# Optimization experiments

Measured on AMD Instinct MI355X. Metric: run time of the kernel, lower is better.

## Reference

```python
import jax, jax.numpy as jnp
import numpy as np

E = 64          # num_routed_experts
K = 6           # num_experts_per_token
NS = 2          # num_shared_experts
D = 512         # hidden_size
F = 512         # expert_intermediate_size = intermediate_size // 4


def setup_inputs() -> dict:
    key = jax.random.key(0)
    ks = jax.random.split(key, 8)
    s = 0.02
    return {
        "hidden_states": jax.random.normal(ks[0], (2, 1024, D), dtype=jnp.float32),
        "Wr": jax.random.normal(ks[1], (D, E), dtype=jnp.float32) * s,      # router
        "sWg": jax.random.normal(ks[2], (NS, D, F), dtype=jnp.float32) * s,  # shared gate_proj
        "sWu": jax.random.normal(ks[3], (NS, D, F), dtype=jnp.float32) * s,  # shared up_proj
        "sWd": jax.random.normal(ks[4], (NS, F, D), dtype=jnp.float32) * s,  # shared down_proj
        "Wg": jax.random.normal(ks[5], (E, D, F), dtype=jnp.float32) * s,    # routed gate_proj
        "Wu": jax.random.normal(ks[6], (E, D, F), dtype=jnp.float32) * s,    # routed up_proj
        "Wd": jax.random.normal(ks[7], (E, F, D), dtype=jnp.float32) * s,    # routed down_proj
    }


def _swiglu_ffn(x, wg, wu, wd):
    # x: (N, D); wg/wu: (D, F); wd: (F, D)
    return (jax.nn.silu(x @ wg) * (x @ wu)) @ wd


def reference(hidden_states, Wr, sWg, sWu, sWd, Wg, Wu, Wd):
    B, S, d = hidden_states.shape
    x = hidden_states.reshape(-1, d)  # (N, D)
    N = x.shape[0]

    # ---- shared experts (always on) ----
    shared = jnp.zeros_like(x)
    for e in range(NS):
        shared = shared + _swiglu_ffn(x, sWg[e], sWu[e], sWd[e])

    # ---- top-k router ----
    logits = x @ Wr                                   # (N, E)
    probs = jax.nn.softmax(logits, axis=-1)
    top_w, top_i = jax.lax.top_k(probs, K)            # (N, K)
    top_w = top_w / jnp.sum(top_w, axis=-1, keepdims=True)  # renormalize
    gate = jnp.zeros((N, E), dtype=x.dtype).at[jnp.arange(N)[:, None], top_i].set(top_w)

    # ---- routed experts: per-expert FFN, combined with sparse gate ----
    routed = jnp.zeros_like(x)
    for e in range(E):
        routed = routed + _swiglu_ffn(x, Wg[e], Wu[e], Wd[e]) * gate[:, e:e + 1]

    out = (shared + routed + x).reshape(B, S, d)
    return out
```

## Files before the change

### kernel.cpp

```cpp
#include <hip/hip_runtime.h>

#define N_TOK 2048
#define DD 512
#define FF 512
#define EE 64
#define TK 6
#define NG 66
#define RSLOT 12288
#define NSLOT 16384
#define BM 64
#define BN 64
#define NKT2 16
#define MAXT 320
#define MATSZ 262144

typedef float f32x4 __attribute__((ext_vector_type(4)));
typedef __bf16 bf16x8 __attribute__((ext_vector_type(8)));

__device__ __forceinline__ unsigned cvtpk(float lo, float hi) {
  unsigned r;
  asm("v_cvt_pk_bf16_f32 %0, %1, %2" : "=v"(r) : "v"(lo), "v"(hi));
  return r;
}

__device__ __forceinline__ int swz4(int r) { return (r + (r >> 2)) & 3; }

__device__ __forceinline__ void gll16(const void* g, void* l) {
  __builtin_amdgcn_global_load_lds(
      (const __attribute__((address_space(1))) unsigned int*)g,
      (__attribute__((address_space(3))) unsigned int*)l, 16, 0, 0);
}

__device__ __forceinline__ void fence_barrier() {
  asm volatile("" ::: "memory");
  __builtin_amdgcn_s_barrier();
  __builtin_amdgcn_sched_barrier(0);
}

__global__ __launch_bounds__(256) void convw_k(
    const float* __restrict__ Wg, const float* __restrict__ Wu, const float* __restrict__ Wd,
    const float* __restrict__ sWg, const float* __restrict__ sWu, const float* __restrict__ sWd,
    short* __restrict__ Wt) {
  __shared__ float T[64][33];
  int y = blockIdx.y;
  int kind = y / 66, idx = y % 66;
  const float* src;
  if (kind == 0)      src = (idx < EE) ? Wg + (size_t)idx * MATSZ : sWg + (size_t)(idx - EE) * MATSZ;
  else if (kind == 1) src = (idx < EE) ? Wu + (size_t)idx * MATSZ : sWu + (size_t)(idx - EE) * MATSZ;
  else                src = (idx < EE) ? Wd + (size_t)idx * MATSZ : sWd + (size_t)(idx - EE) * MATSZ;
  short* dst = Wt + (size_t)y * MATSZ;
  int d0 = (blockIdx.x & 7) * 64;
  int f0 = (blockIdx.x >> 3) * 32;
  int t = threadIdx.x;

  int r = t >> 3, fo = (t & 7) * 4;
  const float* sp = src + (size_t)(d0 + r) * 512 + f0 + fo;
  *(f32x4*)&T[r][fo]      = *(const f32x4*)sp;
  *(f32x4*)&T[r + 32][fo] = *(const f32x4*)(sp + (size_t)32 * 512);
  __syncthreads();

  int f = t >> 3, a = t & 7, dd = a * 8;
  float v[8];
#pragma unroll
  for (int i = 0; i < 8; ++i) v[i] = T[dd + i][f];
  uint4 o;
  o.x = cvtpk(v[0], v[1]); o.y = cvtpk(v[2], v[3]);
  o.z = cvtpk(v[4], v[5]); o.w = cvtpk(v[6], v[7]);
  *(uint4*)&dst[(size_t)(f0 + f) * 512 + d0 + dd] = o;
}

__global__ void convx_k(const float* __restrict__ x, short* __restrict__ Xb) {
  int i = blockIdx.x * 256 + threadIdx.x;
  const f32x4* p = (const f32x4*)(x + (size_t)i * 8);
  f32x4 v0 = p[0], v1 = p[1];
  uint4 o;
  o.x = cvtpk(v0[0], v0[1]); o.y = cvtpk(v0[2], v0[3]);
  o.z = cvtpk(v1[0], v1[1]); o.w = cvtpk(v1[2], v1[3]);
  *(uint4*)&Xb[(size_t)i * 8] = o;
}

__global__ __launch_bounds__(256) void router_k(
    const float* __restrict__ x, const float* __restrict__ Wr,
    int* __restrict__ top_i, float* __restrict__ top_w, int* __restrict__ cnt) {
  __shared__ float xs[16 * 512];
  __shared__ float part[4][16][64];
  int tid = threadIdx.x, lane = tid & 63, w = tid >> 6;
  int t0 = blockIdx.x * 16;
  const f32x4* xin = (const f32x4*)(x + (size_t)t0 * DD);
  f32x4* xs4 = (f32x4*)xs;
#pragma unroll
  for (int i = 0; i < 8; ++i) xs4[i * 256 + tid] = xin[i * 256 + tid];
  __syncthreads();
  float acc[16];
#pragma unroll
  for (int t = 0; t < 16; ++t) acc[t] = 0.f;
  for (int kk = 0; kk < 32; ++kk) {
    int k = w * 128 + kk * 4;
    float w0 = Wr[(size_t)(k + 0) * EE + lane];
    float w1 = Wr[(size_t)(k + 1) * EE + lane];
    float w2 = Wr[(size_t)(k + 2) * EE + lane];
    float w3 = Wr[(size_t)(k + 3) * EE + lane];
#pragma unroll
    for (int t = 0; t < 16; ++t) {
      f32x4 xv = *(const f32x4*)&xs[t * 512 + k];
      acc[t] = fmaf(xv[0], w0, acc[t]);
      acc[t] = fmaf(xv[1], w1, acc[t]);
      acc[t] = fmaf(xv[2], w2, acc[t]);
      acc[t] = fmaf(xv[3], w3, acc[t]);
    }
  }
#pragma unroll
  for (int t = 0; t < 16; ++t) part[w][t][lane] = acc[t];
  __syncthreads();
#pragma unroll
  for (int tt = 0; tt < 4; ++tt) {
    int t = w * 4 + tt;
    float l0 = part[0][t][lane] + part[1][t][lane] + part[2][t][lane] + part[3][t][lane];
    float m = l0;
#pragma unroll
    for (int s = 32; s; s >>= 1) m = fmaxf(m, __shfl_xor(m, s));
    float p = __expf(l0 - m);
    int wi[TK]; float wv[TK];
#pragma unroll
    for (int it = 0; it < TK; ++it) {
      float v = p;
#pragma unroll
      for (int s = 32; s; s >>= 1) v = fmaxf(v, __shfl_xor(v, s));
      unsigned long long b = __ballot(p == v);
      int idx = __ffsll((unsigned long long)b) - 1;
      wi[it] = idx; wv[it] = v;
      if (lane == idx) p = -1.f;
    }
    float wsum = 0.f;
#pragma unroll
    for (int it = 0; it < TK; ++it) wsum += wv[it];
    int tg = t0 + t;
    if (lane < TK) {
      int si = 0; float sv = 0.f;
#pragma unroll
      for (int it = 0; it < TK; ++it) if (lane == it) { si = wi[it]; sv = wv[it]; }
      top_i[tg * TK + lane] = si;
      top_w[tg * TK + lane] = sv / wsum;
      atomicAdd(&cnt[si], 1);
    }
  }
}

__global__ void offsets_k(const int* __restrict__ cnt, int* __restrict__ goff,
                          int* __restrict__ fill, int* __restrict__ wk_g,
                          int* __restrict__ wk_mt, int* __restrict__ nitems) {
  int i = threadIdx.x;
  fill[i] = 0;
  int c = cnt[i];
  int s = c;
#pragma unroll
  for (int d = 1; d < 64; d <<= 1) { int t = __shfl_up(s, d); if (i >= d) s += t; }
  goff[i] = s - c;
  if (i == 63) {
    goff[EE] = RSLOT;
    goff[EE + 1] = RSLOT + N_TOK;
    goff[EE + 2] = RSLOT + 2 * N_TOK;
  }
  int nt = (c + BM - 1) >> 6;
  int ts = nt;
#pragma unroll
  for (int d = 1; d < 64; d <<= 1) { int t = __shfl_up(ts, d); if (i >= d) ts += t; }
  int texcl = ts - nt;
  for (int t = 0; t < nt; ++t) { wk_g[texcl + t] = i; wk_mt[texcl + t] = t; }
  int tot = __shfl(ts, 63);
  wk_g[tot + i] = EE + (i >> 5);
  wk_mt[tot + i] = i & 31;
  if (i == 0) nitems[0] = tot + 64;
}

__global__ void scatter_k(const int* __restrict__ top_i, const float* __restrict__ top_w,
                          const int* __restrict__ goff, int* __restrict__ fill,
                          int* __restrict__ btok, float* __restrict__ bw,
                          int* __restrict__ tslot) {
  int idx = blockIdx.x * blockDim.x + threadIdx.x;
  if (idx < RSLOT) {
    int e = top_i[idx];
    int pos = goff[e] + atomicAdd(&fill[e], 1);
    btok[pos] = idx / TK;
    bw[pos] = top_w[idx];
    tslot[idx] = pos;
  } else if (idx < NSLOT) {
    int j = idx - RSLOT;
    btok[idx] = j & (N_TOK - 1);
    bw[idx] = 1.0f;
  }
}

__global__ __launch_bounds__(256) void gemm1_k(
    const short* __restrict__ Xb, const short* __restrict__ Wtg, const short* __restrict__ Wtu,
    const int* __restrict__ goff, const int* __restrict__ btok,
    const int* __restrict__ wk_g, const int* __restrict__ wk_mt,
    const int* __restrict__ nitems, short* __restrict__ H) {
  int item = blockIdx.y;
  if (item >= nitems[0]) return;
  int g = wk_g[item], mt = wk_mt[item];
  int s0g = goff[g], cnt = goff[g + 1] - s0g;
  int n0 = blockIdx.x * BN;
  const short* gmat = Wtg + (size_t)g * MATSZ;
  const short* umat = Wtu + (size_t)g * MATSZ;

  __shared__ __align__(16) short lds[2][6144];

  int tid = threadIdx.x, lane = tid & 63, w = tid >> 6;
  int wr = w >> 1, wc = w & 1;
  int lr = lane & 15, lgq = lane >> 4;
  int s0 = s0g + mt * BM;

  const short* sp[3];
  int ldst[3];
#pragma unroll
  for (int q = 0; q < 3; ++q) {
    int c = w * 3 + q;
    int mat = c >> 2, cc = c & 3;
    ldst[q] = mat * 2048 + cc * 512;
    int rl = cc * 16 + (lane >> 2);
    int gu = (lane & 3) ^ swz4(rl);
    if (mat == 0) {
      int slot = (mt * BM + rl < cnt) ? s0 + rl : s0;
      sp[q] = Xb + (size_t)btok[slot] * 512 + gu * 8;
    } else if (mat == 1) {
      sp[q] = gmat + (size_t)(n0 + rl) * 512 + gu * 8;
    } else {
      sp[q] = umat + (size_t)(n0 + rl) * 512 + gu * 8;
    }
  }

  f32x4 accg[2][2], accu[2][2];
#pragma unroll
  for (int i = 0; i < 2; ++i)
#pragma unroll
    for (int j = 0; j < 2; ++j) {
      accg[i][j] = f32x4{0.f, 0.f, 0.f, 0.f};
      accu[i][j] = f32x4{0.f, 0.f, 0.f, 0.f};
    }

  auto STAGE = [&](int b, int kt) {
#pragma unroll
    for (int q = 0; q < 3; ++q) gll16(sp[q] + kt * 32, &lds[b][ldst[q]]);
  };
  auto COMPUTE = [&](int b) {
    const short* L = lds[b];
    bf16x8 af[2], bg[2], bu[2];
#pragma unroll
    for (int i = 0; i < 2; ++i) {
      int row = wr * 32 + i * 16 + lr;
      af[i] = *(const bf16x8*)&L[row * 32 + ((lgq ^ swz4(row)) * 8)];
    }
#pragma unroll
    for (int j = 0; j < 2; ++j) {
      int fr = wc * 32 + j * 16 + lr;
      int o = fr * 32 + ((lgq ^ swz4(fr)) * 8);
      bg[j] = *(const bf16x8*)&L[2048 + o];
      bu[j] = *(const bf16x8*)&L[4096 + o];
    }
#pragma unroll
    for (int i = 0; i < 2; ++i)
#pragma unroll
      for (int j = 0; j < 2; ++j) {
        accg[i][j] = __builtin_amdgcn_mfma_f32_16x16x32_bf16(af[i], bg[j], accg[i][j], 0, 0, 0);
        accu[i][j] = __builtin_amdgcn_mfma_f32_16x16x32_bf16(af[i], bu[j], accu[i][j], 0, 0, 0);
      }
  };

  STAGE(0, 0);
  asm volatile("s_waitcnt vmcnt(0)" ::: "memory");
  fence_barrier();
#pragma unroll 1
  for (int kt = 0; kt < NKT2; ++kt) {
    int cur = kt & 1;
    if (kt + 1 < NKT2) STAGE(cur ^ 1, kt + 1);
    COMPUTE(cur);
    if (kt + 1 < NKT2) asm volatile("s_waitcnt vmcnt(0)" ::: "memory");
    fence_barrier();
  }

#pragma unroll
  for (int i = 0; i < 2; ++i)
#pragma unroll
    for (int j = 0; j < 2; ++j)
#pragma unroll
      for (int r = 0; r < 4; ++r) {
        int mrow = wr * 32 + i * 16 + lgq * 4 + r;
        if (mt * BM + mrow < cnt) {
          float gg = accg[i][j][r];
          float uu = accu[i][j][r];
          float hv = (gg / (1.f + __expf(-gg))) * uu;
          int col = n0 + wc * 32 + j * 16 + lr;
          H[(size_t)(s0 + mrow) * FF + col] = (short)(cvtpk(hv, hv) & 0xffffu);
        }
      }
}

__global__ __launch_bounds__(256) void gemm2_k(
    const short* __restrict__ H, const short* __restrict__ Wtd,
    const int* __restrict__ goff, const float* __restrict__ bw,
    const int* __restrict__ wk_g, const int* __restrict__ wk_mt,
    const int* __restrict__ nitems, short* __restrict__ Osl) {
  int item = blockIdx.y;
  if (item >= nitems[0]) return;
  int g = wk_g[item], mt = wk_mt[item];
  int s0g = goff[g], cnt = goff[g + 1] - s0g;
  int n0 = blockIdx.x * BN;
  const short* dmat = Wtd + (size_t)g * MATSZ;

  __shared__ __align__(16) short lds[2][4096];

  int tid = threadIdx.x, lane = tid & 63, w = tid >> 6;
  int wr = w >> 1, wc = w & 1;
  int lr = lane & 15, lgq = lane >> 4;
  int s0 = s0g + mt * BM;

  const short* sp[2];
  int ldst[2];
#pragma unroll
  for (int q = 0; q < 2; ++q) {
    int c = w * 2 + q;
    int mat = c >> 2, cc = c & 3;
    ldst[q] = mat * 2048 + cc * 512;
    int rl = cc * 16 + (lane >> 2);
    int gu = (lane & 3) ^ swz4(rl);
    if (mat == 0) {
      int slot = (mt * BM + rl < cnt) ? s0 + rl : s0;
      sp[q] = H + (size_t)slot * 512 + gu * 8;
    } else {
      sp[q] = dmat + (size_t)(n0 + rl) * 512 + gu * 8;
    }
  }

  f32x4 acc[2][2];
#pragma unroll
  for (int i = 0; i < 2; ++i)
#pragma unroll
    for (int j = 0; j < 2; ++j) acc[i][j] = f32x4{0.f, 0.f, 0.f, 0.f};

  auto STAGE = [&](int b, int kt) {
#pragma unroll
    for (int q = 0; q < 2; ++q) gll16(sp[q] + kt * 32, &lds[b][ldst[q]]);
  };
  auto COMPUTE = [&](int b) {
    const short* L = lds[b];
    bf16x8 af[2], bd[2];
#pragma unroll
    for (int i = 0; i < 2; ++i) {
      int row = wr * 32 + i * 16 + lr;
      af[i] = *(const bf16x8*)&L[row * 32 + ((lgq ^ swz4(row)) * 8)];
    }
#pragma unroll
    for (int j = 0; j < 2; ++j) {
      int dr = wc * 32 + j * 16 + lr;
      bd[j] = *(const bf16x8*)&L[2048 + dr * 32 + ((lgq ^ swz4(dr)) * 8)];
    }
#pragma unroll
    for (int i = 0; i < 2; ++i)
#pragma unroll
      for (int j = 0; j < 2; ++j)
        acc[i][j] = __builtin_amdgcn_mfma_f32_16x16x32_bf16(af[i], bd[j], acc[i][j], 0, 0, 0);
  };

  STAGE(0, 0);
  asm volatile("s_waitcnt vmcnt(0)" ::: "memory");
  fence_barrier();
#pragma unroll 1
  for (int kt = 0; kt < NKT2; ++kt) {
    int cur = kt & 1;
    if (kt + 1 < NKT2) STAGE(cur ^ 1, kt + 1);
    COMPUTE(cur);
    if (kt + 1 < NKT2) asm volatile("s_waitcnt vmcnt(0)" ::: "memory");
    fence_barrier();
  }

#pragma unroll
  for (int i = 0; i < 2; ++i)
#pragma unroll
    for (int r = 0; r < 4; ++r) {
      int mrow = wr * 32 + i * 16 + lgq * 4 + r;
      if (mt * BM + mrow < cnt) {
        int slot = s0 + mrow;
        float wv = bw[slot];
#pragma unroll
        for (int j = 0; j < 2; ++j) {
          int col = n0 + wc * 32 + j * 16 + lr;
          Osl[(size_t)slot * DD + col] = (short)(cvtpk(acc[i][j][r] * wv, 0.f) & 0xffffu);
        }
      }
    }
}

__global__ __launch_bounds__(256) void combine_k(
    const short* __restrict__ Osl, const float* __restrict__ x,
    const int* __restrict__ tslot, float* __restrict__ out) {
  int wv = threadIdx.x >> 6, lane = threadIdx.x & 63;
  int t = blockIdx.x * 4 + wv;
  int d0 = lane * 8;
  const float* xp = x + (size_t)t * DD + d0;
  f32x4 sa = *(const f32x4*)xp;
  f32x4 sb = *(const f32x4*)(xp + 4);
  int slots[8];
#pragma unroll
  for (int k = 0; k < 6; ++k) slots[k] = tslot[t * TK + k];
  slots[6] = RSLOT + t;
  slots[7] = RSLOT + N_TOK + t;
#pragma unroll
  for (int k = 0; k < 8; ++k) {
    uint4 hv = *(const uint4*)&Osl[(size_t)slots[k] * DD + d0];
    unsigned u[4] = {hv.x, hv.y, hv.z, hv.w};
#pragma unroll
    for (int q = 0; q < 4; ++q) {
      float lo = __builtin_bit_cast(float, u[q] << 16);
      float hi = __builtin_bit_cast(float, u[q] & 0xffff0000u);
      if (q < 2) { sa[q * 2] += lo; sa[q * 2 + 1] += hi; }
      else { sb[(q - 2) * 2] += lo; sb[(q - 2) * 2 + 1] += hi; }
    }
  }
  float* op = out + (size_t)t * DD + d0;
  *(f32x4*)op = sa;
  *(f32x4*)(op + 4) = sb;
}

extern "C" void kernel_launch(void* const* d_in, const int* in_sizes, int n_in,
                              void* d_out, int out_size, void* d_ws, size_t ws_size,
                              hipStream_t stream) {
  const float* x   = (const float*)d_in[0];
  const float* Wr  = (const float*)d_in[1];
  const float* sWg = (const float*)d_in[2];
  const float* sWu = (const float*)d_in[3];
  const float* sWd = (const float*)d_in[4];
  const float* Wg  = (const float*)d_in[5];
  const float* Wu  = (const float*)d_in[6];
  const float* Wd  = (const float*)d_in[7];
  float* out = (float*)d_out;

  char* wsb = (char*)d_ws;
  size_t off = 0;
  short* Wt = (short*)(wsb + off);    off += (size_t)198 * MATSZ * 2;
  short* H  = (short*)(wsb + off);    off += (size_t)NSLOT * FF * 2;
  short* Osl = (short*)(wsb + off);   off += (size_t)NSLOT * DD * 2;
  short* Xb = (short*)(wsb + off);    off += (size_t)N_TOK * DD * 2;
  int*   top_i = (int*)(wsb + off);   off += (size_t)RSLOT * 4;
  float* top_w = (float*)(wsb + off); off += (size_t)RSLOT * 4;
  int*   btok = (int*)(wsb + off);    off += (size_t)NSLOT * 4;
  float* bwt  = (float*)(wsb + off);  off += (size_t)NSLOT * 4;
  int*   tslot = (int*)(wsb + off);   off += (size_t)RSLOT * 4;
  int*   cnt  = (int*)(wsb + off);    off += 256;
  int*   fill = (int*)(wsb + off);    off += 256;
  int*   goff = (int*)(wsb + off);    off += 512;
  int*   wk_g = (int*)(wsb + off);    off += MAXT * 4;
  int*   wk_mt = (int*)(wsb + off);   off += MAXT * 4;
  int*   nitems = (int*)(wsb + off);  off += 256;

  const short* Wtg = Wt;
  const short* Wtu = Wt + (size_t)66 * MATSZ;
  const short* Wtd = Wt + (size_t)132 * MATSZ;

  hipMemsetAsync(cnt, 0, 256, stream);
  convw_k<<<dim3(128, 198), 256, 0, stream>>>(Wg, Wu, Wd, sWg, sWu, sWd, Wt);
  convx_k<<<512, 256, 0, stream>>>(x, Xb);
  router_k<<<N_TOK / 16, 256, 0, stream>>>(x, Wr, top_i, top_w, cnt);
  offsets_k<<<1, 64, 0, stream>>>(cnt, goff, fill, wk_g, wk_mt, nitems);
  scatter_k<<<NSLOT / 256, 256, 0, stream>>>(top_i, top_w, goff, fill, btok, bwt, tslot);
  dim3 grid1(FF / BN, MAXT, 1);
  gemm1_k<<<grid1, 256, 0, stream>>>(Xb, Wtg, Wtu, goff, btok, wk_g, wk_mt, nitems, H);
  dim3 grid2(DD / BN, MAXT, 1);
  gemm2_k<<<grid2, 256, 0, stream>>>(H, Wtd, goff, bwt, wk_g, wk_mt, nitems, Osl);
  combine_k<<<N_TOK / 4, 256, 0, stream>>>(Osl, x, tslot, out);
}
```

Before: 220.3 us.

## Enlarge grouped-GEMM M tile to 128 and pipeline weight conversion via LDS

The grouped expert GEMMs now use 128-row M tiles, with each wave owning 32 rows and all 64 columns. This halves the number of work items and reuses each weight tile across twice as many tokens. The offsets kernel and the shared-expert work list are rebuilt for the new tile size, and blocks with no valid rows exit early. The weight transpose/convert kernel is also reworked so each block handles 128 F columns, using async global-to-LDS loads double-buffered with an XOR swizzle. In exchange, accumulator register use is higher and tail padding waste grows for experts with few tokens.

```diff
diff --git a/kernel.cpp b/kernel.cpp
--- a/kernel.cpp
+++ b/kernel.cpp
@@ -8,10 +8,9 @@
 #define NG 66
 #define RSLOT 12288
 #define NSLOT 16384
-#define BM 64
-#define BN 64
+#define BM1 128
 #define NKT2 16
-#define MAXT 320
+#define MAXT 192
 #define MATSZ 262144
 
 typedef float f32x4 __attribute__((ext_vector_type(4)));
@@ -31,17 +30,11 @@
       (__attribute__((address_space(3))) unsigned int*)l, 16, 0, 0);
 }
 
-__device__ __forceinline__ void fence_barrier() {
-  asm volatile("" ::: "memory");
-  __builtin_amdgcn_s_barrier();
-  __builtin_amdgcn_sched_barrier(0);
-}
-
 __global__ __launch_bounds__(256) void convw_k(
     const float* __restrict__ Wg, const float* __restrict__ Wu, const float* __restrict__ Wd,
     const float* __restrict__ sWg, const float* __restrict__ sWu, const float* __restrict__ sWd,
     short* __restrict__ Wt) {
-  __shared__ float T[64][33];
+  __shared__ __align__(16) float B[2][2048];
   int y = blockIdx.y;
   int kind = y / 66, idx = y % 66;
   const float* src;
@@ -50,23 +43,47 @@
   else                src = (idx < EE) ? Wd + (size_t)idx * MATSZ : sWd + (size_t)(idx - EE) * MATSZ;
   short* dst = Wt + (size_t)y * MATSZ;
   int d0 = (blockIdx.x & 7) * 64;
-  int f0 = (blockIdx.x >> 3) * 32;
-  int t = threadIdx.x;
-
-  int r = t >> 3, fo = (t & 7) * 4;
-  const float* sp = src + (size_t)(d0 + r) * 512 + f0 + fo;
-  *(f32x4*)&T[r][fo]      = *(const f32x4*)sp;
-  *(f32x4*)&T[r + 32][fo] = *(const f32x4*)(sp + (size_t)32 * 512);
-  __syncthreads();
-
-  int f = t >> 3, a = t & 7, dd = a * 8;
-  float v[8];
-#pragma unroll
-  for (int i = 0; i < 8; ++i) v[i] = T[dd + i][f];
-  uint4 o;
-  o.x = cvtpk(v[0], v[1]); o.y = cvtpk(v[2], v[3]);
-  o.z = cvtpk(v[4], v[5]); o.w = cvtpk(v[6], v[7]);
-  *(uint4*)&dst[(size_t)(f0 + f) * 512 + d0 + dd] = o;
+  int fp = (blockIdx.x >> 3) * 128;
+  int t = threadIdx.x, lane = t & 63, w = t >> 6;
+
+  int sd[2], su[2];
+#pragma unroll
+  for (int q = 0; q < 2; ++q) {
+    sd[q] = w * 16 + q * 8 + (lane >> 3);
+    su[q] = (lane & 7) ^ (w * 2 + q);
+  }
+  int f = t >> 3, db = (t & 7) * 8;
+  int elem = (((f >> 2) ^ (t & 7)) << 2) | (f & 3);
+
+  auto STAGE = [&](int b, int ft) {
+    int fb = fp + ft * 32;
+#pragma unroll
+    for (int q = 0; q < 2; ++q)
+      gll16(src + (size_t)(d0 + sd[q]) * 512 + fb + su[q] * 4,
+            &B[b][(w * 16 + q * 8) * 32]);
+  };
+
+  STAGE(0, 0);
+#pragma unroll 1
+  for (int ft = 0; ft < 4; ++ft) {
+    int cur = ft & 1;
+    if (ft + 1 < 4) {
+      STAGE(cur ^ 1, ft + 1);
+      asm volatile("s_waitcnt vmcnt(2)" ::: "memory");
+    } else {
+      asm volatile("s_waitcnt vmcnt(0)" ::: "memory");
+    }
+    __builtin_amdgcn_s_barrier();
+    __builtin_amdgcn_sched_barrier(0);
+    float v[8];
+#pragma unroll
+    for (int i = 0; i < 8; ++i) v[i] = B[cur][(db + i) * 32 + elem];
+    uint4 o;
+    o.x = cvtpk(v[0], v[1]); o.y = cvtpk(v[2], v[3]);
+    o.z = cvtpk(v[4], v[5]); o.w = cvtpk(v[6], v[7]);
+    *(uint4*)&dst[(size_t)(fp + ft * 32 + f) * 512 + d0 + db] = o;
+    __builtin_amdgcn_s_barrier();
+  }
 }
 
 __global__ void convx_k(const float* __restrict__ x, short* __restrict__ Xb) {
@@ -161,16 +178,18 @@
     goff[EE + 1] = RSLOT + N_TOK;
     goff[EE + 2] = RSLOT + 2 * N_TOK;
   }
-  int nt = (c + BM - 1) >> 6;
+  int nt = (c + BM1 - 1) >> 7;
   int ts = nt;
 #pragma unroll
   for (int d = 1; d < 64; d <<= 1) { int t = __shfl_up(ts, d); if (i >= d) ts += t; }
   int texcl = ts - nt;
   for (int t = 0; t < nt; ++t) { wk_g[texcl + t] = i; wk_mt[texcl + t] = t; }
   int tot = __shfl(ts, 63);
-  wk_g[tot + i] = EE + (i >> 5);
-  wk_mt[tot + i] = i & 31;
-  if (i == 0) nitems[0] = tot + 64;
+  if (i < 32) {
+    wk_g[tot + i] = EE + (i >> 4);
+    wk_mt[tot + i] = i & 15;
+  }
+  if (i == 0) nitems[0] = tot + 32;
 }
 
 __global__ void scatter_k(const int* __restrict__ top_i, const float* __restrict__ top_w,
@@ -200,68 +219,76 @@
   if (item >= nitems[0]) return;
   int g = wk_g[item], mt = wk_mt[item];
   int s0g = goff[g], cnt = goff[g + 1] - s0g;
-  int n0 = blockIdx.x * BN;
+  if (mt * BM1 >= cnt) return;
+  int n0 = blockIdx.x * 64;
   const short* gmat = Wtg + (size_t)g * MATSZ;
   const short* umat = Wtu + (size_t)g * MATSZ;
 
-  __shared__ __align__(16) short lds[2][6144];
+  __shared__ __align__(16) short lds[2][8192];
 
   int tid = threadIdx.x, lane = tid & 63, w = tid >> 6;
-  int wr = w >> 1, wc = w & 1;
   int lr = lane & 15, lgq = lane >> 4;
-  int s0 = s0g + mt * BM;
-
-  const short* sp[3];
-  int ldst[3];
-#pragma unroll
-  for (int q = 0; q < 3; ++q) {
-    int c = w * 3 + q;
-    int mat = c >> 2, cc = c & 3;
-    ldst[q] = mat * 2048 + cc * 512;
-    int rl = cc * 16 + (lane >> 2);
-    int gu = (lane & 3) ^ swz4(rl);
-    if (mat == 0) {
-      int slot = (mt * BM + rl < cnt) ? s0 + rl : s0;
+  int s0 = s0g + mt * BM1;
+
+  const short* sp[4];
+  int ldst[4];
+#pragma unroll
+  for (int q = 0; q < 4; ++q) {
+    int c = w * 4 + q;
+    int rl, gu;
+    if (c < 8) {
+      rl = c * 16 + (lane >> 2);
+      gu = (lane & 3) ^ swz4(rl);
+      ldst[q] = c * 512;
+      int slot = (mt * BM1 + rl < cnt) ? s0 + rl : s0;
       sp[q] = Xb + (size_t)btok[slot] * 512 + gu * 8;
-    } else if (mat == 1) {
+    } else if (c < 12) {
+      int cc = c - 8;
+      rl = cc * 16 + (lane >> 2);
+      gu = (lane & 3) ^ swz4(rl);
+      ldst[q] = 4096 + cc * 512;
       sp[q] = gmat + (size_t)(n0 + rl) * 512 + gu * 8;
     } else {
+      int cc = c - 12;
+      rl = cc * 16 + (lane >> 2);
+      gu = (lane & 3) ^ swz4(rl);
+      ldst[q] = 6144 + cc * 512;
       sp[q] = umat + (size_t)(n0 + rl) * 512 + gu * 8;
     }
   }
 
-  f32x4 accg[2][2], accu[2][2];
+  f32x4 accg[2][4], accu[2][4];
 #pragma unroll
   for (int i = 0; i < 2; ++i)
 #pragma unroll
-    for (int j = 0; j < 2; ++j) {
+    for (int j = 0; j < 4; ++j) {
       accg[i][j] = f32x4{0.f, 0.f, 0.f, 0.f};
       accu[i][j] = f32x4{0.f, 0.f, 0.f, 0.f};
     }
 
   auto STAGE = [&](int b, int kt) {
 #pragma unroll
-    for (int q = 0; q < 3; ++q) gll16(sp[q] + kt * 32, &lds[b][ldst[q]]);
+    for (int q = 0; q < 4; ++q) gll16(sp[q] + kt * 32, &lds[b][ldst[q]]);
   };
   auto COMPUTE = [&](int b) {
     const short* L = lds[b];
-    bf16x8 af[2], bg[2], bu[2];
+    bf16x8 af[2], bg[4], bu[4];
 #pragma unroll
     for (int i = 0; i < 2; ++i) {
-      int row = wr * 32 + i * 16 + lr;
+      int row = w * 32 + i * 16 + lr;
       af[i] = *(const bf16x8*)&L[row * 32 + ((lgq ^ swz4(row)) * 8)];
     }
 #pragma unroll
-    for (int j = 0; j < 2; ++j) {
-      int fr = wc * 32 + j * 16 + lr;
+    for (int j = 0; j < 4; ++j) {
+      int fr = j * 16 + lr;
       int o = fr * 32 + ((lgq ^ swz4(fr)) * 8);
-      bg[j] = *(const bf16x8*)&L[2048 + o];
-      bu[j] = *(const bf16x8*)&L[4096 + o];
+      bg[j] = *(const bf16x8*)&L[4096 + o];
+      bu[j] = *(const bf16x8*)&L[6144 + o];
     }
 #pragma unroll
     for (int i = 0; i < 2; ++i)
 #pragma unroll
-      for (int j = 0; j < 2; ++j) {
+      for (int j = 0; j < 4; ++j) {
         accg[i][j] = __builtin_amdgcn_mfma_f32_16x16x32_bf16(af[i], bg[j], accg[i][j], 0, 0, 0);
         accu[i][j] = __builtin_amdgcn_mfma_f32_16x16x32_bf16(af[i], bu[j], accu[i][j], 0, 0, 0);
       }
@@ -269,28 +296,30 @@
 
   STAGE(0, 0);
   asm volatile("s_waitcnt vmcnt(0)" ::: "memory");
-  fence_barrier();
+  __builtin_amdgcn_s_barrier();
+  __builtin_amdgcn_sched_barrier(0);
 #pragma unroll 1
   for (int kt = 0; kt < NKT2; ++kt) {
     int cur = kt & 1;
     if (kt + 1 < NKT2) STAGE(cur ^ 1, kt + 1);
     COMPUTE(cur);
-    if (kt + 1 < NKT2) asm volatile("s_waitcnt vmcnt(0)" ::: "memory");
-    fence_barrier();
+    asm volatile("s_waitcnt vmcnt(0)" ::: "memory");
+    __builtin_amdgcn_s_barrier();
+    __builtin_amdgcn_sched_barrier(0);
   }
 
 #pragma unroll
   for (int i = 0; i < 2; ++i)
 #pragma unroll
-    for (int j = 0; j < 2; ++j)
+    for (int j = 0; j < 4; ++j)
 #pragma unroll
       for (int r = 0; r < 4; ++r) {
-        int mrow = wr * 32 + i * 16 + lgq * 4 + r;
-        if (mt * BM + mrow < cnt) {
+        int mrow = w * 32 + i * 16 + lgq * 4 + r;
+        if (mt * BM1 + mrow < cnt) {
           float gg = accg[i][j][r];
           float uu = accu[i][j][r];
           float hv = (gg / (1.f + __expf(-gg))) * uu;
-          int col = n0 + wc * 32 + j * 16 + lr;
+          int col = n0 + j * 16 + lr;
           H[(size_t)(s0 + mrow) * FF + col] = (short)(cvtpk(hv, hv) & 0xffffu);
         }
       }
@@ -305,86 +334,92 @@
   if (item >= nitems[0]) return;
   int g = wk_g[item], mt = wk_mt[item];
   int s0g = goff[g], cnt = goff[g + 1] - s0g;
-  int n0 = blockIdx.x * BN;
+  if (mt * BM1 >= cnt) return;
+  int n0 = blockIdx.x * 64;
   const short* dmat = Wtd + (size_t)g * MATSZ;
 
-  __shared__ __align__(16) short lds[2][4096];
+  __shared__ __align__(16) short lds[2][6144];
 
   int tid = threadIdx.x, lane = tid & 63, w = tid >> 6;
-  int wr = w >> 1, wc = w & 1;
   int lr = lane & 15, lgq = lane >> 4;
-  int s0 = s0g + mt * BM;
-
-  const short* sp[2];
-  int ldst[2];
-#pragma unroll
-  for (int q = 0; q < 2; ++q) {
-    int c = w * 2 + q;
-    int mat = c >> 2, cc = c & 3;
-    ldst[q] = mat * 2048 + cc * 512;
-    int rl = cc * 16 + (lane >> 2);
-    int gu = (lane & 3) ^ swz4(rl);
-    if (mat == 0) {
-      int slot = (mt * BM + rl < cnt) ? s0 + rl : s0;
+  int s0 = s0g + mt * BM1;
+
+  const short* sp[3];
+  int ldst[3];
+#pragma unroll
+  for (int q = 0; q < 3; ++q) {
+    int c = w * 3 + q;
+    int rl, gu;
+    if (c < 8) {
+      rl = c * 16 + (lane >> 2);
+      gu = (lane & 3) ^ swz4(rl);
+      ldst[q] = c * 512;
+      int slot = (mt * BM1 + rl < cnt) ? s0 + rl : s0;
       sp[q] = H + (size_t)slot * 512 + gu * 8;
     } else {
+      int cc = c - 8;
+      rl = cc * 16 + (lane >> 2);
+      gu = (lane & 3) ^ swz4(rl);
+      ldst[q] = 4096 + cc * 512;
       sp[q] = dmat + (size_t)(n0 + rl) * 512 + gu * 8;
     }
   }
 
-  f32x4 acc[2][2];
+  f32x4 acc[2][4];
 #pragma unroll
   for (int i = 0; i < 2; ++i)
 #pragma unroll
-    for (int j = 0; j < 2; ++j) acc[i][j] = f32x4{0.f, 0.f, 0.f, 0.f};
+    for (int j = 0; j < 4; ++j) acc[i][j] = f32x4{0.f, 0.f, 0.f, 0.f};
 
   auto STAGE = [&](int b, int kt) {
 #pragma unroll
-    for (int q = 0; q < 2; ++q) gll16(sp[q] + kt * 32, &lds[b][ldst[q]]);
+    for (int q = 0; q < 3; ++q) gll16(sp[q] + kt * 32, &lds[b][ldst[q]]);
   };
   auto COMPUTE = [&](int b) {
     const short* L = lds[b];
-    bf16x8 af[2], bd[2];
+    bf16x8 af[2], bd[4];
 #pragma unroll
     for (int i = 0; i < 2; ++i) {
-      int row = wr * 32 + i * 16 + lr;
+      int row = w * 32 + i * 16 + lr;
       af[i] = *(const bf16x8*)&L[row * 32 + ((lgq ^ swz4(row)) * 8)];
     }
 #pragma unroll
-    for (int j = 0; j < 2; ++j) {
-      int dr = wc * 32 + j * 16 + lr;
-      bd[j] = *(const bf16x8*)&L[2048 + dr * 32 + ((lgq ^ swz4(dr)) * 8)];
+    for (int j = 0; j < 4; ++j) {
+      int dr = j * 16 + lr;
+      bd[j] = *(const bf16x8*)&L[4096 + dr * 32 + ((lgq ^ swz4(dr)) * 8)];
     }
 #pragma unroll
     for (int i = 0; i < 2; ++i)
 #pragma unroll
-      for (int j = 0; j < 2; ++j)
+      for (int j = 0; j < 4; ++j)
         acc[i][j] = __builtin_amdgcn_mfma_f32_16x16x32_bf16(af[i], bd[j], acc[i][j], 0, 0, 0);
   };
 
   STAGE(0, 0);
   asm volatile("s_waitcnt vmcnt(0)" ::: "memory");
-  fence_barrier();
+  __builtin_amdgcn_s_barrier();
+  __builtin_amdgcn_sched_barrier(0);
 #pragma unroll 1
   for (int kt = 0; kt < NKT2; ++kt) {
     int cur = kt & 1;
     if (kt + 1 < NKT2) STAGE(cur ^ 1, kt + 1);
     COMPUTE(cur);
-    if (kt + 1 < NKT2) asm volatile("s_waitcnt vmcnt(0)" ::: "memory");
-    fence_barrier();
+    asm volatile("s_waitcnt vmcnt(0)" ::: "memory");
+    __builtin_amdgcn_s_barrier();
+    __builtin_amdgcn_sched_barrier(0);
   }
 
 #pragma unroll
   for (int i = 0; i < 2; ++i)
 #pragma unroll
     for (int r = 0; r < 4; ++r) {
-      int mrow = wr * 32 + i * 16 + lgq * 4 + r;
-      if (mt * BM + mrow < cnt) {
+      int mrow = w * 32 + i * 16 + lgq * 4 + r;
+      if (mt * BM1 + mrow < cnt) {
         int slot = s0 + mrow;
         float wv = bw[slot];
 #pragma unroll
-        for (int j = 0; j < 2; ++j) {
-          int col = n0 + wc * 32 + j * 16 + lr;
+        for (int j = 0; j < 4; ++j) {
+          int col = n0 + j * 16 + lr;
           Osl[(size_t)slot * DD + col] = (short)(cvtpk(acc[i][j][r] * wv, 0.f) & 0xffffu);
         }
       }
@@ -458,14 +493,14 @@
   const short* Wtd = Wt + (size_t)132 * MATSZ;
 
   hipMemsetAsync(cnt, 0, 256, stream);
-  convw_k<<<dim3(128, 198), 256, 0, stream>>>(Wg, Wu, Wd, sWg, sWu, sWd, Wt);
+  convw_k<<<dim3(32, 198), 256, 0, stream>>>(Wg, Wu, Wd, sWg, sWu, sWd, Wt);
   convx_k<<<512, 256, 0, stream>>>(x, Xb);
   router_k<<<N_TOK / 16, 256, 0, stream>>>(x, Wr, top_i, top_w, cnt);
   offsets_k<<<1, 64, 0, stream>>>(cnt, goff, fill, wk_g, wk_mt, nitems);
   scatter_k<<<NSLOT / 256, 256, 0, stream>>>(top_i, top_w, goff, fill, btok, bwt, tslot);
-  dim3 grid1(FF / BN, MAXT, 1);
+  dim3 grid1(FF / 64, MAXT, 1);
   gemm1_k<<<grid1, 256, 0, stream>>>(Xb, Wtg, Wtu, goff, btok, wk_g, wk_mt, nitems, H);
-  dim3 grid2(DD / BN, MAXT, 1);
+  dim3 grid2(DD / 64, MAXT, 1);
   gemm2_k<<<grid2, 256, 0, stream>>>(H, Wtd, goff, bwt, wk_g, wk_mt, nitems, Osl);
   combine_k<<<N_TOK / 4, 256, 0, stream>>>(Osl, x, tslot, out);
 }
```

After: 220.0 us. Within noise of the previous version (-0.1%).
